# Performance work log

Hardware: AMD Instinct MI355X
Metric: run time of the kernel (lower is better)

## Reference

```python
import jax, jax.numpy as jnp
import numpy as np

BIT = 8
Q_MAX = float(2 ** BIT - 1)  # 255
SMOOTH = 0.999


def hardsigmoid(x):
    # torch nn.Hardsigmoid: relu6(x + 3) / 6
    return jnp.clip(x / 6.0 + 0.5, 0.0, 1.0)


def setup_inputs() -> dict:
    key = jax.random.key(0)
    ks = jax.random.split(key, 5)
    B, C, H, W = 64, 256, 56, 56
    Cs = 64  # _make_divisible(256 // 4, 8)
    x = jax.random.normal(ks[0], (B, C, H, W), jnp.float32)
    w1 = jax.random.normal(ks[1], (Cs, C), jnp.float32) * 0.05  # fc1 1x1 conv weight
    b1 = jax.random.normal(ks[2], (Cs,), jnp.float32) * 0.05
    w2 = jax.random.normal(ks[3], (C, Cs), jnp.float32) * 0.05  # fc2 1x1 conv weight
    b2 = jax.random.normal(ks[4], (C,), jnp.float32) * 0.05
    act_range = jnp.array([-1.0, 1.0], jnp.float32)  # EMA-tracked (min, max) buffer
    return {"x": x, "w1": w1, "b1": b1, "w2": w2, "b2": b2, "act_range": act_range}


def reference(x, w1, b1, w2, b2, act_range):
    # squeeze: adaptive_avg_pool2d(input, 1) -> [B, C]
    pooled = jnp.mean(x, axis=(2, 3))
    # fc1: 1x1 conv + bias + ReLU
    h = jax.nn.relu(jnp.einsum('bc,sc->bs', pooled, w1) + b1)
    # fc2: 1x1 conv + bias, then quantized Hardsigmoid gate
    g = hardsigmoid(jnp.einsum('bs,cs->bc', h, w2) + b2)
    out = x * g[:, :, None, None]
    # training path: EMA min/max update + fake quantization (STE)
    rmin = jnp.min(out)
    rmax = jnp.max(out)
    new_min = act_range[0] * SMOOTH + rmin * (1.0 - SMOOTH)
    new_max = act_range[1] * SMOOTH + rmax * (1.0 - SMOOTH)
    s = (new_max - new_min) / Q_MAX
    z = -jnp.round(new_min / s)
    s = jax.lax.stop_gradient(s)
    z = jax.lax.stop_gradient(z)
    q = (jnp.clip(jnp.round(out / s + z), 0.0, Q_MAX) - z) * s
    # straight-through estimator
    return out + jax.lax.stop_gradient(q - out)
```

## Files before the change

### kernel.cpp

```cpp
#include <hip/hip_runtime.h>
#include <hip/hip_bf16.h>

#define B_   64
#define C_   256
#define BC   (B_ * C_)
#define CS   64
#define HW   3136
#define HW4  784

typedef float floatx4 __attribute__((ext_vector_type(4)));

__device__ __forceinline__ float fmin4(float4 v) {
    return fminf(fminf(v.x, v.y), fminf(v.z, v.w));
}
__device__ __forceinline__ float fmax4(float4 v) {
    return fmaxf(fmaxf(v.x, v.y), fmaxf(v.z, v.w));
}

__global__ __launch_bounds__(256) void k_pool(const float* __restrict__ x,
                                              float* __restrict__ pooled,
                                              float* __restrict__ xmn,
                                              float* __restrict__ xmx) {
    const int bc = blockIdx.x;
    const float4* xp = (const float4*)(x + (size_t)bc * HW);
    const int t = threadIdx.x;

    float sum = 0.0f;
    float mn = 3.402823466e38f;
    float mx = -3.402823466e38f;
    for (int i = t; i < HW4; i += 256) {
        float4 v = xp[i];
        sum += (v.x + v.y) + (v.z + v.w);
        mn = fminf(mn, fmin4(v));
        mx = fmaxf(mx, fmax4(v));
    }
    for (int off = 32; off > 0; off >>= 1) {
        sum += __shfl_down(sum, off, 64);
        mn = fminf(mn, __shfl_down(mn, off, 64));
        mx = fmaxf(mx, __shfl_down(mx, off, 64));
    }
    __shared__ float ssum[4], smn[4], smx[4];
    const int wave = t >> 6, lane = t & 63;
    if (lane == 0) { ssum[wave] = sum; smn[wave] = mn; smx[wave] = mx; }
    __syncthreads();
    if (t == 0) {
        float S  = (ssum[0] + ssum[1]) + (ssum[2] + ssum[3]);
        float MN = fminf(fminf(smn[0], smn[1]), fminf(smn[2], smn[3]));
        float MX = fmaxf(fmaxf(smx[0], smx[1]), fmaxf(smx[2], smx[3]));
        pooled[bc] = S / (float)HW;
        xmn[bc] = MN;
        xmx[bc] = MX;
    }
}

__global__ __launch_bounds__(256) void k_fc1(const float* __restrict__ pooled,
                                             const float* __restrict__ w1,
                                             const float* __restrict__ b1,
                                             float* __restrict__ h) {
    const int b = blockIdx.x;
    const int t = threadIdx.x;
    __shared__ float p[C_];
    __shared__ float part[4][CS];
    p[t] = pooled[b * C_ + t];
    __syncthreads();

    const int s = t & 63, q = t >> 6;
    const float4* wr = (const float4*)(w1 + s * C_ + q * 64);
    const float4* pr = (const float4*)(p + q * 64);
    float acc = 0.0f;
    #pragma unroll
    for (int k = 0; k < 16; ++k) {
        float4 w = wr[k], pv = pr[k];
        acc += w.x * pv.x + w.y * pv.y + w.z * pv.z + w.w * pv.w;
    }
    part[q][s] = acc;
    __syncthreads();
    if (t < CS) {
        float a = (part[0][t] + part[1][t]) + (part[2][t] + part[3][t]) + b1[t];
        h[b * CS + t] = fmaxf(a, 0.0f);
    }
}

__global__ __launch_bounds__(256) void k_fc2(const float* __restrict__ h,
                                             const float* __restrict__ xmn,
                                             const float* __restrict__ xmx,
                                             const float* __restrict__ w2,
                                             const float* __restrict__ b2,
                                             float* __restrict__ g,
                                             float* __restrict__ pmn,
                                             float* __restrict__ pmx) {
    const int b = blockIdx.x;
    const int t = threadIdx.x;
    __shared__ float hs[CS];
    if (t < CS) hs[t] = h[b * CS + t];
    __syncthreads();

    const float4* wr = (const float4*)(w2 + t * CS);
    const float4* hr = (const float4*)hs;
    float acc = b2[t];
    #pragma unroll
    for (int k = 0; k < 16; ++k) {
        float4 w = wr[k], hv = hr[k];
        acc += w.x * hv.x + w.y * hv.y + w.z * hv.z + w.w * hv.w;
    }
    float gg = fminf(fmaxf(acc / 6.0f + 0.5f, 0.0f), 1.0f);
    const int i = b * C_ + t;
    g[i] = gg;
    float mn = gg * xmn[i];
    float mx = gg * xmx[i];
    for (int off = 32; off > 0; off >>= 1) {
        mn = fminf(mn, __shfl_down(mn, off, 64));
        mx = fmaxf(mx, __shfl_down(mx, off, 64));
    }
    __shared__ float smn[4], smx[4];
    const int wave = t >> 6, lane = t & 63;
    if (lane == 0) { smn[wave] = mn; smx[wave] = mx; }
    __syncthreads();
    if (t == 0) {
        pmn[b] = fminf(fminf(smn[0], smn[1]), fminf(smn[2], smn[3]));
        pmx[b] = fmaxf(fmaxf(smx[0], smx[1]), fmaxf(smx[2], smx[3]));
    }
}

__global__ __launch_bounds__(64) void k_sz(const float* __restrict__ pmn,
                                           const float* __restrict__ pmx,
                                           const float* __restrict__ act_range,
                                           float* __restrict__ sz) {
    const int t = threadIdx.x;
    float mn = pmn[t];
    float mx = pmx[t];
    for (int off = 32; off > 0; off >>= 1) {
        mn = fminf(mn, __shfl_down(mn, off, 64));
        mx = fmaxf(mx, __shfl_down(mx, off, 64));
    }
    if (t == 0) {
        float new_min = act_range[0] * 0.999f + mn * 0.001f;
        float new_max = act_range[1] * 0.999f + mx * 0.001f;
        float s = (new_max - new_min) / 255.0f;
        float z = -rintf(new_min / s);
        sz[0] = s;
        sz[1] = z;
        sz[2] = 1.0f / s;
    }
}

__device__ __forceinline__ float quant1(float o, float s, float z, float inv_s) {
    float q = rintf(__builtin_fmaf(o, inv_s, z));
    q = fminf(fmaxf(q, 0.0f), 255.0f);
    return (q - z) * s;
}

__global__ __launch_bounds__(256) void k_quant(const float* __restrict__ x,
                                               const float* __restrict__ g,
                                               const float* __restrict__ sz,
                                               float* __restrict__ out) {
    const int bc = blockIdx.x;
    const float gv = g[bc];
    const float s = sz[0];
    const float z = sz[1];
    const float inv_s = sz[2];
    const float4* xp = (const float4*)(x + (size_t)bc * HW);
    floatx4* op = (floatx4*)(out + (size_t)bc * HW);
    const int t = threadIdx.x;
    for (int i = t; i < HW4; i += 256) {
        float4 v = xp[i];
        floatx4 r;
        r.x = quant1(v.x * gv, s, z, inv_s);
        r.y = quant1(v.y * gv, s, z, inv_s);
        r.z = quant1(v.z * gv, s, z, inv_s);
        r.w = quant1(v.w * gv, s, z, inv_s);
        __builtin_nontemporal_store(r, op + i);
    }
}

extern "C" void kernel_launch(void* const* d_in, const int* in_sizes, int n_in,
                              void* d_out, int out_size, void* d_ws, size_t ws_size,
                              hipStream_t stream) {
    const float* x         = (const float*)d_in[0];
    const float* w1        = (const float*)d_in[1];
    const float* b1        = (const float*)d_in[2];
    const float* w2        = (const float*)d_in[3];
    const float* b2        = (const float*)d_in[4];
    const float* act_range = (const float*)d_in[5];
    float* out = (float*)d_out;

    float* ws     = (float*)d_ws;
    float* pooled = ws;
    float* xmn    = ws + BC;
    float* xmx    = ws + 2 * BC;
    float* g      = ws + 3 * BC;
    float* h      = ws + 4 * BC;
    float* pmn    = h + B_ * CS;
    float* pmx    = pmn + B_;
    float* sz     = pmx + B_;

    k_pool <<<BC, 256, 0, stream>>>(x, pooled, xmn, xmx);
    k_fc1  <<<B_, 256, 0, stream>>>(pooled, w1, b1, h);
    k_fc2  <<<B_, 256, 0, stream>>>(h, xmn, xmx, w2, b2, g, pmn, pmx);
    k_sz   <<<1, 64, 0, stream>>>(pmn, pmx, act_range, sz);
    k_quant<<<BC, 256, 0, stream>>>(x, g, sz, out);
}
```

Baseline: 383.5 us.

## Fuse fc1/fc2 and scale kernels, assign one wave per channel

Merges the fc1 and fc2 kernels into one block-per-batch kernel and folds the scale/zero-point computation into every wave of the quant kernel, cutting five launches to three. The pool and quant kernels now map one 64-lane wave to each (b,c) plane with a fully unrolled loop, removing the shared-memory cross-wave reduction and __syncthreads. Each quant wave redundantly reduces the 64 per-batch min/max values, which adds a small amount of work per block.

```diff
diff --git a/kernel.cpp b/kernel.cpp
--- a/kernel.cpp
+++ b/kernel.cpp
@@ -1,5 +1,4 @@
 #include <hip/hip_runtime.h>
-#include <hip/hip_bf16.h>
 
 #define B_   64
 #define C_   256
@@ -7,6 +6,8 @@
 #define CS   64
 #define HW   3136
 #define HW4  784
+#define HW4F 768
+#define HW4T 16
 
 typedef float floatx4 __attribute__((ext_vector_type(4)));
 
@@ -21,15 +22,22 @@
                                               float* __restrict__ pooled,
                                               float* __restrict__ xmn,
                                               float* __restrict__ xmx) {
-    const int bc = blockIdx.x;
+    const int wave = threadIdx.x >> 6, lane = threadIdx.x & 63;
+    const int bc = blockIdx.x * 4 + wave;
     const float4* xp = (const float4*)(x + (size_t)bc * HW);
-    const int t = threadIdx.x;
 
     float sum = 0.0f;
     float mn = 3.402823466e38f;
     float mx = -3.402823466e38f;
-    for (int i = t; i < HW4; i += 256) {
-        float4 v = xp[i];
+    #pragma unroll
+    for (int k = 0; k < 12; ++k) {
+        float4 v = xp[lane + k * 64];
+        sum += (v.x + v.y) + (v.z + v.w);
+        mn = fminf(mn, fmin4(v));
+        mx = fmaxf(mx, fmax4(v));
+    }
+    if (lane < HW4T) {
+        float4 v = xp[HW4F + lane];
         sum += (v.x + v.y) + (v.z + v.w);
         mn = fminf(mn, fmin4(v));
         mx = fmaxf(mx, fmax4(v));
@@ -39,65 +47,53 @@
         mn = fminf(mn, __shfl_down(mn, off, 64));
         mx = fmaxf(mx, __shfl_down(mx, off, 64));
     }
-    __shared__ float ssum[4], smn[4], smx[4];
-    const int wave = t >> 6, lane = t & 63;
-    if (lane == 0) { ssum[wave] = sum; smn[wave] = mn; smx[wave] = mx; }
-    __syncthreads();
-    if (t == 0) {
-        float S  = (ssum[0] + ssum[1]) + (ssum[2] + ssum[3]);
-        float MN = fminf(fminf(smn[0], smn[1]), fminf(smn[2], smn[3]));
-        float MX = fmaxf(fmaxf(smx[0], smx[1]), fmaxf(smx[2], smx[3]));
-        pooled[bc] = S / (float)HW;
-        xmn[bc] = MN;
-        xmx[bc] = MX;
+    if (lane == 0) {
+        pooled[bc] = sum / (float)HW;
+        xmn[bc] = mn;
+        xmx[bc] = mx;
     }
 }
 
-__global__ __launch_bounds__(256) void k_fc1(const float* __restrict__ pooled,
+__global__ __launch_bounds__(256) void k_mid(const float* __restrict__ pooled,
                                              const float* __restrict__ w1,
                                              const float* __restrict__ b1,
-                                             float* __restrict__ h) {
-    const int b = blockIdx.x;
-    const int t = threadIdx.x;
-    __shared__ float p[C_];
-    __shared__ float part[4][CS];
-    p[t] = pooled[b * C_ + t];
-    __syncthreads();
-
-    const int s = t & 63, q = t >> 6;
-    const float4* wr = (const float4*)(w1 + s * C_ + q * 64);
-    const float4* pr = (const float4*)(p + q * 64);
-    float acc = 0.0f;
-    #pragma unroll
-    for (int k = 0; k < 16; ++k) {
-        float4 w = wr[k], pv = pr[k];
-        acc += w.x * pv.x + w.y * pv.y + w.z * pv.z + w.w * pv.w;
-    }
-    part[q][s] = acc;
-    __syncthreads();
-    if (t < CS) {
-        float a = (part[0][t] + part[1][t]) + (part[2][t] + part[3][t]) + b1[t];
-        h[b * CS + t] = fmaxf(a, 0.0f);
-    }
-}
-
-__global__ __launch_bounds__(256) void k_fc2(const float* __restrict__ h,
+                                             const float* __restrict__ w2,
+                                             const float* __restrict__ b2,
                                              const float* __restrict__ xmn,
                                              const float* __restrict__ xmx,
-                                             const float* __restrict__ w2,
-                                             const float* __restrict__ b2,
                                              float* __restrict__ g,
                                              float* __restrict__ pmn,
                                              float* __restrict__ pmx) {
     const int b = blockIdx.x;
     const int t = threadIdx.x;
-    __shared__ float hs[CS];
-    if (t < CS) hs[t] = h[b * CS + t];
+    __shared__ __align__(16) float p[C_];
+    __shared__ __align__(16) float part[4][CS];
+    __shared__ __align__(16) float hs[CS];
+    p[t] = pooled[b * C_ + t];
     __syncthreads();
 
+    {
+        const int s_ = t & 63, q = t >> 6;
+        const float4* wr = (const float4*)(w1 + s_ * C_ + q * 64);
+        const float4* pr = (const float4*)(p + q * 64);
+        float acc = 0.0f;
+        #pragma unroll
+        for (int k = 0; k < 16; ++k) {
+            float4 w = wr[k], pv = pr[k];
+            acc += w.x * pv.x + w.y * pv.y + w.z * pv.z + w.w * pv.w;
+        }
+        part[q][s_] = acc;
+    }
+    __syncthreads();
+    if (t < CS) {
+        float a = (part[0][t] + part[1][t]) + (part[2][t] + part[3][t]) + b1[t];
+        hs[t] = fmaxf(a, 0.0f);
+    }
+    __syncthreads();
+
+    float acc = b2[t];
     const float4* wr = (const float4*)(w2 + t * CS);
     const float4* hr = (const float4*)hs;
-    float acc = b2[t];
     #pragma unroll
     for (int k = 0; k < 16; ++k) {
         float4 w = wr[k], hv = hr[k];
@@ -122,28 +118,6 @@
     }
 }
 
-__global__ __launch_bounds__(64) void k_sz(const float* __restrict__ pmn,
-                                           const float* __restrict__ pmx,
-                                           const float* __restrict__ act_range,
-                                           float* __restrict__ sz) {
-    const int t = threadIdx.x;
-    float mn = pmn[t];
-    float mx = pmx[t];
-    for (int off = 32; off > 0; off >>= 1) {
-        mn = fminf(mn, __shfl_down(mn, off, 64));
-        mx = fmaxf(mx, __shfl_down(mx, off, 64));
-    }
-    if (t == 0) {
-        float new_min = act_range[0] * 0.999f + mn * 0.001f;
-        float new_max = act_range[1] * 0.999f + mx * 0.001f;
-        float s = (new_max - new_min) / 255.0f;
-        float z = -rintf(new_min / s);
-        sz[0] = s;
-        sz[1] = z;
-        sz[2] = 1.0f / s;
-    }
-}
-
 __device__ __forceinline__ float quant1(float o, float s, float z, float inv_s) {
     float q = rintf(__builtin_fmaf(o, inv_s, z));
     q = fminf(fmaxf(q, 0.0f), 255.0f);
@@ -152,17 +126,42 @@
 
 __global__ __launch_bounds__(256) void k_quant(const float* __restrict__ x,
                                                const float* __restrict__ g,
-                                               const float* __restrict__ sz,
+                                               const float* __restrict__ pmn,
+                                               const float* __restrict__ pmx,
+                                               const float* __restrict__ act_range,
                                                float* __restrict__ out) {
-    const int bc = blockIdx.x;
+    const int wave = threadIdx.x >> 6, lane = threadIdx.x & 63;
+
+    float mn = pmn[lane];
+    float mx = pmx[lane];
+    for (int off = 32; off > 0; off >>= 1) {
+        mn = fminf(mn, __shfl_xor(mn, off, 64));
+        mx = fmaxf(mx, __shfl_xor(mx, off, 64));
+    }
+    const float new_min = act_range[0] * 0.999f + mn * 0.001f;
+    const float new_max = act_range[1] * 0.999f + mx * 0.001f;
+    const float s = (new_max - new_min) / 255.0f;
+    const float z = -rintf(new_min / s);
+    const float inv_s = 1.0f / s;
+
+    const int bc = blockIdx.x * 4 + wave;
     const float gv = g[bc];
-    const float s = sz[0];
-    const float z = sz[1];
-    const float inv_s = sz[2];
     const float4* xp = (const float4*)(x + (size_t)bc * HW);
     floatx4* op = (floatx4*)(out + (size_t)bc * HW);
-    const int t = threadIdx.x;
-    for (int i = t; i < HW4; i += 256) {
+
+    #pragma unroll
+    for (int k = 0; k < 12; ++k) {
+        const int i = lane + k * 64;
+        float4 v = xp[i];
+        floatx4 r;
+        r.x = quant1(v.x * gv, s, z, inv_s);
+        r.y = quant1(v.y * gv, s, z, inv_s);
+        r.z = quant1(v.z * gv, s, z, inv_s);
+        r.w = quant1(v.w * gv, s, z, inv_s);
+        __builtin_nontemporal_store(r, op + i);
+    }
+    if (lane < HW4T) {
+        const int i = HW4F + lane;
         float4 v = xp[i];
         floatx4 r;
         r.x = quant1(v.x * gv, s, z, inv_s);
@@ -189,14 +188,10 @@
     float* xmn    = ws + BC;
     float* xmx    = ws + 2 * BC;
     float* g      = ws + 3 * BC;
-    float* h      = ws + 4 * BC;
-    float* pmn    = h + B_ * CS;
+    float* pmn    = ws + 4 * BC;
     float* pmx    = pmn + B_;
-    float* sz     = pmx + B_;
 
-    k_pool <<<BC, 256, 0, stream>>>(x, pooled, xmn, xmx);
-    k_fc1  <<<B_, 256, 0, stream>>>(pooled, w1, b1, h);
-    k_fc2  <<<B_, 256, 0, stream>>>(h, xmn, xmx, w2, b2, g, pmn, pmx);
-    k_sz   <<<1, 64, 0, stream>>>(pmn, pmx, act_range, sz);
-    k_quant<<<BC, 256, 0, stream>>>(x, g, sz, out);
+    k_pool <<<BC / 4, 256, 0, stream>>>(x, pooled, xmn, xmx);
+    k_mid  <<<B_,     256, 0, stream>>>(pooled, w1, b1, w2, b2, xmn, xmx, g, pmn, pmx);
+    k_quant<<<BC / 4, 256, 0, stream>>>(x, g, pmn, pmx, act_range, out);
 }
```

Measured after the change: 384.3 us, median of 2. About the same (+0.2%).
